# Optimization experiments

Measured on AMD Instinct MI355X. Metric: run time of the kernel, lower is better.

The kernel has to match this reference:

```python
import jax, jax.numpy as jnp
import numpy as np

N_NODES = 100000
N_EDGES = 1600000
D_IN = 32
D_OUT = 32


def setup_inputs() -> dict:
    key = jax.random.key(0)
    ks = jax.random.split(key, 5)
    feat = jax.random.normal(ks[0], (N_NODES, D_IN), dtype=jnp.float32)
    # xavier_uniform with relu gain, shape (out, in)
    gain = float(np.sqrt(2.0))
    bound = gain * float(np.sqrt(6.0 / (D_IN + D_OUT)))
    W_self = jax.random.uniform(ks[1], (D_OUT, D_IN), minval=-bound, maxval=bound, dtype=jnp.float32)
    W_neigh = jax.random.uniform(ks[2], (D_OUT, D_IN), minval=-bound, maxval=bound, dtype=jnp.float32)
    b_neigh = jnp.zeros((D_OUT,), dtype=jnp.float32)
    src = jax.random.randint(ks[3], (N_EDGES,), 0, N_NODES)
    dst = jax.random.randint(ks[4], (N_EDGES,), 0, N_NODES)
    return {"feat": feat, "W_self": W_self, "W_neigh": W_neigh,
            "b_neigh": b_neigh, "src": src, "dst": dst}


def reference(feat, W_self, W_neigh, b_neigh, src, dst):
    # copy_src + mean aggregation: gather src features, segment-sum into dst,
    # divide by in-degree (0 for isolated dst nodes, matching DGL mean).
    msgs = feat[src]  # [E, D_in] irregular gather
    neigh_sum = jax.ops.segment_sum(msgs, dst, num_segments=N_NODES)  # [N, D_in]
    deg = jax.ops.segment_sum(jnp.ones((dst.shape[0],), feat.dtype), dst,
                              num_segments=N_NODES)  # [N]
    neigh = neigh_sum / jnp.maximum(deg, 1.0)[:, None]
    # GraphSAGE combine: fc_self(h_self) + fc_neigh(neigh)
    rst = feat @ W_self.T + neigh @ W_neigh.T + b_neigh
    return rst
```

## Files before the change

kernel.cpp:

```cpp
#include <hip/hip_runtime.h>

#define D 32
#define SHIFT 7
#define P 128
#define BMAX 1024
#define TILE 4096
#define STHREADS 1024
#define CAP 3072
#define TMAX 512
#define AP 37
#define WP 36

#define FXS 131072.0f
#define FXINV 7.62939453125e-06f

__global__ __launch_bounds__(STHREADS) void scatter_tiles(
        const int* __restrict__ src, const int* __restrict__ dst,
        int* __restrict__ records, int* __restrict__ startsT, int E, int Bn, int T) {
    __shared__ int lhist[STHREADS];
    __shared__ int lofs[BMAX];
    __shared__ int wsum[16];
    __shared__ int stage[TILE];

    int t = threadIdx.x;
    int lane = t & 63;
    int wid = t >> 6;
    int tileStart = blockIdx.x * TILE;

    lhist[t] = 0;
    __syncthreads();

    int sarr[4], darr[4];
    int e0 = tileStart + 4 * t;
    if (tileStart + TILE <= E) {
        int4 s4 = ((const int4*)src)[tileStart / 4 + t];
        int4 d4 = ((const int4*)dst)[tileStart / 4 + t];
        sarr[0] = s4.x; sarr[1] = s4.y; sarr[2] = s4.z; sarr[3] = s4.w;
        darr[0] = d4.x; darr[1] = d4.y; darr[2] = d4.z; darr[3] = d4.w;
    } else {
#pragma unroll
        for (int i = 0; i < 4; ++i) {
            int e = e0 + i;
            sarr[i] = (e < E) ? src[e] : 0;
            darr[i] = (e < E) ? dst[e] : 0;
        }
    }

    int recs[4], bks[4], rr[4];
#pragma unroll
    for (int i = 0; i < 4; ++i) {
        int e = e0 + i;
        if (e < E) {
            int b = darr[i] >> SHIFT;
            recs[i] = (sarr[i] << SHIFT) | (darr[i] & (P - 1));
            bks[i] = b;
            rr[i] = atomicAdd(&lhist[b], 1);
        } else bks[i] = -1;
    }
    __syncthreads();

    int own = lhist[t];
    int v = own;
#pragma unroll
    for (int off = 1; off < 64; off <<= 1) {
        int u = __shfl_up(v, off, 64);
        if (lane >= off) v += u;
    }
    if (lane == 63) wsum[wid] = v;
    __syncthreads();
    if (wid == 0) {
        int s = (lane < 16) ? wsum[lane] : 0;
#pragma unroll
        for (int off = 1; off < 16; off <<= 1) {
            int u = __shfl_up(s, off, 64);
            if (lane >= off) s += u;
        }
        if (lane < 16) wsum[lane] = s;
    }
    __syncthreads();
    int incl = v + (wid ? wsum[wid - 1] : 0);
    int ex = incl - own;
    if (t <= Bn) startsT[(size_t)t * T + blockIdx.x] = ex;
    if (t < Bn) lofs[t] = ex;
    __syncthreads();

#pragma unroll
    for (int i = 0; i < 4; ++i) {
        if (bks[i] >= 0) stage[lofs[bks[i]] + rr[i]] = recs[i];
    }
    __syncthreads();

    int4* dp = reinterpret_cast<int4*>(records + (size_t)tileStart);
    const int4* sp = reinterpret_cast<const int4*>(stage);
    dp[t] = sp[t];
}

__global__ __launch_bounds__(512) void bucket_final(
        const float* __restrict__ feat, const int* __restrict__ records,
        const int* __restrict__ startsT,
        const float* __restrict__ Wself, const float* __restrict__ Wneigh,
        const float* __restrict__ bias, float* __restrict__ out,
        int N, int T, int Bn) {
    __shared__ float4 ubuf[1024];
    __shared__ int sacc[P * AP];
    __shared__ float sWs[D * WP];
    __shared__ float sWn[D * WP];
    __shared__ float sb[D];
    __shared__ int sdeg[P];
    __shared__ int tstart[TMAX];
    __shared__ int tbase[TMAX + 1];
    __shared__ int wsum2[8];

    int* raw = reinterpret_cast<int*>(ubuf);
    float* sfeatF = reinterpret_cast<float*>(ubuf);
    float* saccF = reinterpret_cast<float*>(sacc);

    int b = blockIdx.x;
    int t = threadIdx.x;
    int lane = t & 63;
    int wid = t >> 6;

    float4 fr0 = make_float4(0.f, 0.f, 0.f, 0.f);
    float4 fr1 = fr0;
    {
        int n0 = (b << SHIFT) + (t >> 3);
        int n1 = (b << SHIFT) + ((t + 512) >> 3);
        if (n0 < N) fr0 = ((const float4*)feat)[(size_t)n0 * 8 + (t & 7)];
        if (n1 < N) fr1 = ((const float4*)feat)[(size_t)n1 * 8 + (t & 7)];
    }

    for (int i = t; i < P * AP; i += 512) sacc[i] = 0;
    if (t < P) sdeg[t] = 0;
    for (int i = t; i < D * D; i += 512) {
        int r = i >> 5, c = i & 31;
        sWs[r * WP + c] = Wself[i];
        sWn[r * WP + c] = Wneigh[i];
    }
    if (t < D) sb[t] = bias[t];

    int myc = 0;
    if (t < T) {
        int s0v = startsT[(size_t)b * T + t];
        int s1v = startsT[(size_t)(b + 1) * T + t];
        tstart[t] = s0v;
        myc = s1v - s0v;
    }
    int v = myc;
#pragma unroll
    for (int off = 1; off < 64; off <<= 1) {
        int u = __shfl_up(v, off, 64);
        if (lane >= off) v += u;
    }
    if (lane == 63) wsum2[wid] = v;
    __syncthreads();
    if (wid == 0) {
        int s = (lane < 8) ? wsum2[lane] : 0;
#pragma unroll
        for (int off = 1; off < 8; off <<= 1) {
            int u = __shfl_up(s, off, 64);
            if (lane >= off) s += u;
        }
        if (lane < 8) wsum2[lane] = s;
    }
    __syncthreads();
    int incl = v + (wid ? wsum2[wid - 1] : 0);
    if (t < T) tbase[t] = incl - myc;
    if (t == T - 1) tbase[T] = incl;
    __syncthreads();

    int m = min(tbase[T], CAP);

    int lane4 = t & 3, tg4 = t >> 2;
    for (int tau = tg4; tau < T; tau += 128) {
        int s = tstart[tau];
        int rb = tbase[tau];
        int c2 = tbase[tau + 1] - rb;
        const int* rp = records + (size_t)tau * TILE + s;
        for (int l = lane4; l < c2; l += 4) {
            int pos = rb + l;
            if (pos < CAP) raw[pos] = rp[l];
        }
    }
    __syncthreads();

    int team = t >> 3;
    int part = t & 7;
    for (int base = team; base < m; base += 512) {
        float4 vv[8];
        int nl8[8];
        bool ok[8];
#pragma unroll
        for (int u = 0; u < 8; ++u) {
            int idx = base + 64 * u;
            ok[u] = idx < m;
            int rec = raw[ok[u] ? idx : 0];
            int s = rec >> SHIFT;
            nl8[u] = rec & (P - 1);
            vv[u] = *reinterpret_cast<const float4*>(
                feat + (size_t)s * D + part * 4);
        }
#pragma unroll
        for (int u = 0; u < 8; ++u) {
            if (ok[u]) {
                int* ac = &sacc[nl8[u] * AP + part * 4];
                atomicAdd(ac + 0, __float2int_rn(vv[u].x * FXS));
                atomicAdd(ac + 1, __float2int_rn(vv[u].y * FXS));
                atomicAdd(ac + 2, __float2int_rn(vv[u].z * FXS));
                atomicAdd(ac + 3, __float2int_rn(vv[u].w * FXS));
                if (part == 0) atomicAdd(&sdeg[nl8[u]], 1);
            }
        }
    }
    __syncthreads();

    int rv[8];
#pragma unroll
    for (int r = 0; r < 8; ++r) {
        int i = t + 512 * r;
        rv[r] = sacc[(i >> 5) * AP + (i & 31)];
    }
    __syncthreads();
#pragma unroll
    for (int r = 0; r < 8; ++r) {
        int i = t + 512 * r;
        saccF[i] = (float)rv[r] * FXINV;
    }
    ubuf[t] = fr0;
    ubuf[t + 512] = fr1;
    __syncthreads();

    int j = t & 31;
    int nb = t >> 5;
    const float4* wsr = reinterpret_cast<const float4*>(&sWs[j * WP]);
    const float4* wnr = reinterpret_cast<const float4*>(&sWn[j * WP]);
    float bj = sb[j];
#pragma unroll
    for (int q = 0; q < 8; ++q) {
        int nl = q * 16 + nb;
        int n = (b << SHIFT) + nl;
        if (n >= N) continue;
        const float4* fr = reinterpret_cast<const float4*>(&sfeatF[nl * 32]);
        const float4* nr = reinterpret_cast<const float4*>(&saccF[nl * 32]);
        float accS = 0.f, accN = 0.f;
#pragma unroll
        for (int kk = 0; kk < 8; ++kk) {
            float4 f4 = fr[kk], w4 = wsr[kk];
            accS += f4.x * w4.x + f4.y * w4.y + f4.z * w4.z + f4.w * w4.w;
            float4 n4 = nr[kk], u4 = wnr[kk];
            accN += n4.x * u4.x + n4.y * u4.y + n4.z * u4.z + n4.w * u4.w;
        }
        float inv = 1.0f / (float)max(sdeg[nl], 1);
        out[(size_t)n * D + j] = accS + inv * accN + bj;
    }
}

extern "C" void kernel_launch(void* const* d_in, const int* in_sizes, int n_in,
                              void* d_out, int out_size, void* d_ws, size_t ws_size,
                              hipStream_t stream) {
    const float* feat   = (const float*)d_in[0];
    const float* Wself  = (const float*)d_in[1];
    const float* Wneigh = (const float*)d_in[2];
    const float* bnb    = (const float*)d_in[3];
    const int*   src    = (const int*)d_in[4];
    const int*   dst    = (const int*)d_in[5];

    int N = in_sizes[0] / D;
    int E = in_sizes[4];
    int Bn = (N + P - 1) / P;
    int T  = (E + TILE - 1) / TILE;

    int* records = (int*)d_ws;
    int* startsT = records + (size_t)T * TILE;

    scatter_tiles<<<T, STHREADS, 0, stream>>>(src, dst, records, startsT, E, Bn, T);
    bucket_final<<<Bn, 512, 0, stream>>>(feat, records, startsT, Wself, Wneigh, bnb,
                                         (float*)d_out, N, T, Bn);
}
```

Baseline: 135.0 us.

## Halve scatter tile size, chunk tile prefix scan, register-block the final GEMV

Halves the scatter tile from 4096 to 2048 edges, which doubles the number of scatter blocks (782) for better CU occupancy. Because that count now exceeds 512, the per-bucket prefix scan over tiles in bucket_final becomes a chunked loop with a running base. The final combine is register-tiled: each thread computes 4 nodes by 2 outputs, reusing weight loads, with padded shared rows (stride 36) to reduce bank conflicts. The cost is twice as many start offsets, more per-tile segment reads in bucket_final, and extra scan iterations.

```diff
diff --git a/kernel.cpp b/kernel.cpp
--- a/kernel.cpp
+++ b/kernel.cpp
@@ -4,12 +4,13 @@
 #define SHIFT 7
 #define P 128
 #define BMAX 1024
-#define TILE 4096
+#define TILE 2048
 #define STHREADS 1024
 #define CAP 3072
-#define TMAX 512
+#define TMAX 784
 #define AP 37
 #define WP 36
+#define SF 36
 
 #define FXS 131072.0f
 #define FXINV 7.62939453125e-06f
@@ -30,25 +31,25 @@
     lhist[t] = 0;
     __syncthreads();
 
-    int sarr[4], darr[4];
-    int e0 = tileStart + 4 * t;
+    int sarr[2], darr[2];
+    int e0 = tileStart + 2 * t;
     if (tileStart + TILE <= E) {
-        int4 s4 = ((const int4*)src)[tileStart / 4 + t];
-        int4 d4 = ((const int4*)dst)[tileStart / 4 + t];
-        sarr[0] = s4.x; sarr[1] = s4.y; sarr[2] = s4.z; sarr[3] = s4.w;
-        darr[0] = d4.x; darr[1] = d4.y; darr[2] = d4.z; darr[3] = d4.w;
+        int2 s2 = ((const int2*)src)[tileStart / 2 + t];
+        int2 d2 = ((const int2*)dst)[tileStart / 2 + t];
+        sarr[0] = s2.x; sarr[1] = s2.y;
+        darr[0] = d2.x; darr[1] = d2.y;
     } else {
 #pragma unroll
-        for (int i = 0; i < 4; ++i) {
+        for (int i = 0; i < 2; ++i) {
             int e = e0 + i;
             sarr[i] = (e < E) ? src[e] : 0;
             darr[i] = (e < E) ? dst[e] : 0;
         }
     }
 
-    int recs[4], bks[4], rr[4];
-#pragma unroll
-    for (int i = 0; i < 4; ++i) {
+    int recs[2], bks[2], rr[2];
+#pragma unroll
+    for (int i = 0; i < 2; ++i) {
         int e = e0 + i;
         if (e < E) {
             int b = darr[i] >> SHIFT;
@@ -85,14 +86,16 @@
     __syncthreads();
 
 #pragma unroll
-    for (int i = 0; i < 4; ++i) {
+    for (int i = 0; i < 2; ++i) {
         if (bks[i] >= 0) stage[lofs[bks[i]] + rr[i]] = recs[i];
     }
     __syncthreads();
 
-    int4* dp = reinterpret_cast<int4*>(records + (size_t)tileStart);
-    const int4* sp = reinterpret_cast<const int4*>(stage);
-    dp[t] = sp[t];
+    if (t < TILE / 4) {
+        int4* dp = reinterpret_cast<int4*>(records + (size_t)tileStart);
+        const int4* sp = reinterpret_cast<const int4*>(stage);
+        dp[t] = sp[t];
+    }
 }
 
 __global__ __launch_bounds__(512) void bucket_final(
@@ -101,7 +104,7 @@
         const float* __restrict__ Wself, const float* __restrict__ Wneigh,
         const float* __restrict__ bias, float* __restrict__ out,
         int N, int T, int Bn) {
-    __shared__ float4 ubuf[1024];
+    __shared__ float ubuf[P * SF];
     __shared__ int sacc[P * AP];
     __shared__ float sWs[D * WP];
     __shared__ float sWn[D * WP];
@@ -110,9 +113,10 @@
     __shared__ int tstart[TMAX];
     __shared__ int tbase[TMAX + 1];
     __shared__ int wsum2[8];
+    __shared__ int ctot;
 
     int* raw = reinterpret_cast<int*>(ubuf);
-    float* sfeatF = reinterpret_cast<float*>(ubuf);
+    float* sfeatF = ubuf;
     float* saccF = reinterpret_cast<float*>(sacc);
 
     int b = blockIdx.x;
@@ -138,37 +142,44 @@
     }
     if (t < D) sb[t] = bias[t];
 
-    int myc = 0;
-    if (t < T) {
-        int s0v = startsT[(size_t)b * T + t];
-        int s1v = startsT[(size_t)(b + 1) * T + t];
-        tstart[t] = s0v;
-        myc = s1v - s0v;
-    }
-    int v = myc;
-#pragma unroll
-    for (int off = 1; off < 64; off <<= 1) {
-        int u = __shfl_up(v, off, 64);
-        if (lane >= off) v += u;
-    }
-    if (lane == 63) wsum2[wid] = v;
-    __syncthreads();
-    if (wid == 0) {
-        int s = (lane < 8) ? wsum2[lane] : 0;
-#pragma unroll
-        for (int off = 1; off < 8; off <<= 1) {
-            int u = __shfl_up(s, off, 64);
-            if (lane >= off) s += u;
-        }
-        if (lane < 8) wsum2[lane] = s;
-    }
-    __syncthreads();
-    int incl = v + (wid ? wsum2[wid - 1] : 0);
-    if (t < T) tbase[t] = incl - myc;
-    if (t == T - 1) tbase[T] = incl;
-    __syncthreads();
-
-    int m = min(tbase[T], CAP);
+    int mbase = 0;
+    for (int chunk = 0; chunk < T; chunk += 512) {
+        int tt = chunk + t;
+        int myc = 0;
+        if (tt < T) {
+            int s0v = startsT[(size_t)b * T + tt];
+            int s1v = startsT[(size_t)(b + 1) * T + tt];
+            tstart[tt] = s0v;
+            myc = s1v - s0v;
+        }
+        int v = myc;
+#pragma unroll
+        for (int off = 1; off < 64; off <<= 1) {
+            int u = __shfl_up(v, off, 64);
+            if (lane >= off) v += u;
+        }
+        if (lane == 63) wsum2[wid] = v;
+        __syncthreads();
+        if (wid == 0) {
+            int s = (lane < 8) ? wsum2[lane] : 0;
+#pragma unroll
+            for (int off = 1; off < 8; off <<= 1) {
+                int u = __shfl_up(s, off, 64);
+                if (lane >= off) s += u;
+            }
+            if (lane < 8) wsum2[lane] = s;
+        }
+        __syncthreads();
+        int incl = v + (wid ? wsum2[wid - 1] : 0);
+        if (tt < T) tbase[tt] = mbase + incl - myc;
+        if (t == 511) ctot = incl;
+        __syncthreads();
+        mbase += ctot;
+    }
+    if (t == 0) tbase[T] = mbase;
+    __syncthreads();
+
+    int m = min(mbase, CAP);
 
     int lane4 = t & 3, tg4 = t >> 2;
     for (int tau = tg4; tau < T; tau += 128) {
@@ -223,34 +234,49 @@
 #pragma unroll
     for (int r = 0; r < 8; ++r) {
         int i = t + 512 * r;
-        saccF[i] = (float)rv[r] * FXINV;
-    }
-    ubuf[t] = fr0;
-    ubuf[t + 512] = fr1;
-    __syncthreads();
-
-    int j = t & 31;
-    int nb = t >> 5;
-    const float4* wsr = reinterpret_cast<const float4*>(&sWs[j * WP]);
-    const float4* wnr = reinterpret_cast<const float4*>(&sWn[j * WP]);
-    float bj = sb[j];
-#pragma unroll
-    for (int q = 0; q < 8; ++q) {
-        int nl = q * 16 + nb;
+        saccF[(i >> 5) * SF + (i & 31)] = (float)rv[r] * FXINV;
+    }
+    *reinterpret_cast<float4*>(&sfeatF[(t >> 3) * SF + (t & 7) * 4]) = fr0;
+    *reinterpret_cast<float4*>(&sfeatF[((t + 512) >> 3) * SF + (t & 7) * 4]) = fr1;
+    __syncthreads();
+
+    int jp = t & 15;
+    int nq = t >> 4;
+    int j0 = jp, j1 = jp + 16;
+    float accS[4][2], accN[4][2];
+#pragma unroll
+    for (int i = 0; i < 4; ++i) {
+        accS[i][0] = 0.f; accS[i][1] = 0.f;
+        accN[i][0] = 0.f; accN[i][1] = 0.f;
+    }
+    const float* fb = &sfeatF[(nq * 4) * SF];
+    const float* nb = &saccF[(nq * 4) * SF];
+#pragma unroll 1
+    for (int kk = 0; kk < 8; ++kk) {
+        float4 w0 = *reinterpret_cast<const float4*>(&sWs[j0 * WP + kk * 4]);
+        float4 w1 = *reinterpret_cast<const float4*>(&sWs[j1 * WP + kk * 4]);
+        float4 u0 = *reinterpret_cast<const float4*>(&sWn[j0 * WP + kk * 4]);
+        float4 u1 = *reinterpret_cast<const float4*>(&sWn[j1 * WP + kk * 4]);
+#pragma unroll
+        for (int i = 0; i < 4; ++i) {
+            float4 f4 = *reinterpret_cast<const float4*>(&fb[i * SF + kk * 4]);
+            float4 n4 = *reinterpret_cast<const float4*>(&nb[i * SF + kk * 4]);
+            accS[i][0] += f4.x * w0.x + f4.y * w0.y + f4.z * w0.z + f4.w * w0.w;
+            accS[i][1] += f4.x * w1.x + f4.y * w1.y + f4.z * w1.z + f4.w * w1.w;
+            accN[i][0] += n4.x * u0.x + n4.y * u0.y + n4.z * u0.z + n4.w * u0.w;
+            accN[i][1] += n4.x * u1.x + n4.y * u1.y + n4.z * u1.z + n4.w * u1.w;
+        }
+    }
+    float b0 = sb[j0], b1 = sb[j1];
+#pragma unroll
+    for (int i = 0; i < 4; ++i) {
+        int nl = nq * 4 + i;
         int n = (b << SHIFT) + nl;
-        if (n >= N) continue;
-        const float4* fr = reinterpret_cast<const float4*>(&sfeatF[nl * 32]);
-        const float4* nr = reinterpret_cast<const float4*>(&saccF[nl * 32]);
-        float accS = 0.f, accN = 0.f;
-#pragma unroll
-        for (int kk = 0; kk < 8; ++kk) {
-            float4 f4 = fr[kk], w4 = wsr[kk];
-            accS += f4.x * w4.x + f4.y * w4.y + f4.z * w4.z + f4.w * w4.w;
-            float4 n4 = nr[kk], u4 = wnr[kk];
-            accN += n4.x * u4.x + n4.y * u4.y + n4.z * u4.z + n4.w * u4.w;
-        }
-        float inv = 1.0f / (float)max(sdeg[nl], 1);
-        out[(size_t)n * D + j] = accS + inv * accN + bj;
+        if (n < N) {
+            float inv = 1.0f / (float)max(sdeg[nl], 1);
+            out[(size_t)n * D + j0] = accS[i][0] + inv * accN[i][0] + b0;
+            out[(size_t)n * D + j1] = accS[i][1] + inv * accN[i][1] + b1;
+        }
     }
 }
 
```

Result: slower. 137.9 us (+2.1%).
